# Kernel optimization log

Hardware: AMD Instinct MI355X
Metric: run time of the kernel (lower is better)

The kernel has to match this reference:

```python
import jax, jax.numpy as jnp
import numpy as np


def _bilinear_align_corners(img, H_out, W_out):
    # img: [B, C, h, w] -> [B, C, H_out, W_out], matching F.interpolate(mode='bilinear', align_corners=True)
    b, c, h, w = img.shape
    ys = jnp.linspace(0.0, h - 1.0, H_out)
    xs = jnp.linspace(0.0, w - 1.0, W_out)
    y0 = jnp.floor(ys).astype(jnp.int32)
    x0 = jnp.floor(xs).astype(jnp.int32)
    y1 = jnp.minimum(y0 + 1, h - 1)
    x1 = jnp.minimum(x0 + 1, w - 1)
    wy = (ys - y0)[:, None]          # [H_out, 1]
    wx = (xs - x0)[None, :]          # [1, W_out]

    def gather(yi, xi):
        return img[:, :, yi, :][:, :, :, xi]  # [B, C, H_out, W_out]

    top = gather(y0, x0) * (1.0 - wx) + gather(y0, x1) * wx
    bot = gather(y1, x0) * (1.0 - wx) + gather(y1, x1) * wx
    return top * (1.0 - wy) + bot * wy


def _conv1x1(x, W, b):
    # x: [B, C, H, W_], W: [O, C], b: [O]
    return jnp.einsum('bchw,oc->bohw', x, W) + b[None, :, None, None]


def setup_inputs() -> dict:
    key = jax.random.key(0)
    ks = jax.random.split(key, 9)
    B, C, H, W = 4, 256, 64, 64
    C8 = C // 8
    s_qk = 1.0 / np.sqrt(C)
    return {
        'x': jax.random.normal(ks[0], (B, C, H, W), dtype=jnp.float32),
        'guiding_map0': jax.random.normal(ks[1], (B, 1, 32, 32), dtype=jnp.float32),
        'Wq': jax.random.normal(ks[2], (C8, C), dtype=jnp.float32) * s_qk,
        'bq': jax.random.normal(ks[3], (C8,), dtype=jnp.float32) * 0.01,
        'Wk': jax.random.normal(ks[4], (C8, C), dtype=jnp.float32) * s_qk,
        'bk': jax.random.normal(ks[5], (C8,), dtype=jnp.float32) * 0.01,
        'Wv': jax.random.normal(ks[6], (C, C), dtype=jnp.float32) * s_qk,
        'bv': jax.random.normal(ks[7], (C,), dtype=jnp.float32) * 0.01,
        'gamma': jax.random.normal(ks[8], (1,), dtype=jnp.float32) * 0.1,
    }


def reference(x, guiding_map0, Wq, bq, Wk, bk, Wv, bv, gamma):
    B, C, H, W = x.shape
    N = H * W
    # upsample guiding map to x's spatial size, then sigmoid gate
    gm = jax.nn.sigmoid(_bilinear_align_corners(guiding_map0, H, W))  # [B,1,H,W]
    gate = 1.0 + gm

    q = (_conv1x1(x, Wq, bq) * gate).reshape(B, -1, N)  # [B, C//8, N]
    k = (_conv1x1(x, Wk, bk) * gate).reshape(B, -1, N)  # [B, C//8, N]
    v = (_conv1x1(x, Wv, bv) * gate).reshape(B, C, N)   # [B, C, N]

    # energy[b, n, m] = q[b, :, n] . k[b, :, m]
    energy = jnp.einsum('bcn,bcm->bnm', q, k)           # [B, N, N]
    attention = jax.nn.softmax(energy, axis=-1)
    # out[b, c, n] = sum_m v[b, c, m] * attention[b, n, m]
    out = jnp.einsum('bcm,bnm->bcn', v, attention).reshape(B, C, H, W)
    return gamma[0] * out + x
```

## Files before the change

kernel.cpp:

```cpp
#include <hip/hip_runtime.h>
#include <hip/hip_bf16.h>
#include <cstdint>

typedef __attribute__((ext_vector_type(4)))  float f32x4;
typedef __attribute__((ext_vector_type(16))) float f32x16;
typedef __attribute__((ext_vector_type(8)))  short s16x8;

#define LOG2E 1.4426950408889634f
#define RESC_THR 8.0f

#define B_   4
#define C_   256
#define N_   4096
#define NT_  256
#define MB_  128
#define QG_  128

#define WS_WFRAG 0u
#define WS_BIAS  163840u
#define WS_Q     262144u
#define WS_K     1310720u
#define WS_V     2359296u

__device__ __forceinline__ short bf16s(float f) {
  return (short)__bfloat16_as_ushort(__float2bfloat16(f));
}

__global__ void wprep_kernel(const float* __restrict__ Wq, const float* __restrict__ Wk,
                             const float* __restrict__ Wv, const float* __restrict__ bq,
                             const float* __restrict__ bk, const float* __restrict__ bv,
                             short* __restrict__ wfrag, float* __restrict__ bias) {
  int d0 = blockIdx.x * 256 + threadIdx.x;
  int d = d0;
  int j  = d & 7;  d >>= 3;
  int c  = d & 15; d >>= 4;
  int g  = d & 3;  d >>= 2;
  int ks = d & 7;  d >>= 3;
  int t  = d;
  int o  = t * 16 + c;
  int ch = ks * 32 + g * 8 + j;
  float w = (o < 32) ? Wq[o * 256 + ch] : (o < 64) ? Wk[(o - 32) * 256 + ch]
                                                   : Wv[(o - 64) * 256 + ch];
  wfrag[d0] = bf16s(w);
  if (d0 < 320) bias[d0] = (d0 < 32) ? bq[d0] : (d0 < 64) ? bk[d0 - 32] : bv[d0 - 64];
}

__global__ __launch_bounds__(256) void proj_kernel(
    const float* __restrict__ x, const short* __restrict__ wfrag,
    const float* __restrict__ bias, const float* __restrict__ gm,
    short* __restrict__ qs, short* __restrict__ ksz, short* __restrict__ vs) {
  int b = blockIdx.x >> 8, nt = blockIdx.x & 255;
  int lane = threadIdx.x & 63, wave = threadIdx.x >> 6;
  int g = lane >> 4, c = lane & 15;
  int n = nt * 16 + c;

  float gt;
  {
    int y = n >> 6, xp = n & 63;
    float fy = (float)(y * 31) / 63.0f;
    float fx = (float)(xp * 31) / 63.0f;
    int y0 = (int)fy, x0 = (int)fx;
    float wy = fy - (float)y0, wx = fx - (float)x0;
    int y1 = min(y0 + 1, 31), x1 = min(x0 + 1, 31);
    const float* p = gm + b * 1024;
    float v00 = p[y0 * 32 + x0], v01 = p[y0 * 32 + x1];
    float v10 = p[y1 * 32 + x0], v11 = p[y1 * 32 + x1];
    float top = v00 * (1.f - wx) + v01 * wx;
    float bot = v10 * (1.f - wx) + v11 * wx;
    float gv  = top * (1.f - wy) + bot * wy;
    gt = 1.0f + 1.0f / (1.0f + expf(-gv));
  }

  const float* xb = x + b * (C_ * N_) + n;
  s16x8 xf[8];
  #pragma unroll
  for (int ks = 0; ks < 8; ++ks) {
    int ch0 = ks * 32 + g * 8;
    s16x8 v;
    #pragma unroll
    for (int j = 0; j < 8; ++j) v[j] = bf16s(xb[(ch0 + j) * N_]);
    xf[ks] = v;
  }

  int qt32 = n >> 5, r = n & 31;
  for (int t = wave * 5; t < wave * 5 + 5; ++t) {
    f32x4 acc = {0.f, 0.f, 0.f, 0.f};
    #pragma unroll
    for (int ks = 0; ks < 8; ++ks) {
      s16x8 wf = *(const s16x8*)(wfrag + ((((t * 8 + ks) * 4 + g) * 16 + c) * 8));
      acc = __builtin_amdgcn_mfma_f32_16x16x32_bf16(wf, xf[ks], acc, 0, 0, 0);
    }
    #pragma unroll
    for (int jj = 0; jj < 4; ++jj) {
      int o = t * 16 + g * 4 + jj;
      float val = (acc[jj] + bias[o]) * gt;
      short bv16 = bf16s(val);
      if (o < 64) {
        int ch = o & 31;
        int s  = (ch >> 4) & 1, hi = (ch >> 3) & 1, j = ch & 7;
        short* dst = (o < 32) ? qs : ksz;
        dst[(((b * QG_ + qt32) * 2 + s) * 64 + hi * 32 + r) * 8 + j] = bv16;
      } else {
        int cv = o - 64;
        int ct = cv >> 5, lam = cv & 31;
        int s  = (r >> 4) & 1, r4 = r & 15;
        int k  = (r4 & 3) | (((r4 >> 3) & 1) << 2) | (((r4 >> 2) & 1) << 3);
        int hi = k >> 3, j = k & 7;
        vs[((((size_t)(b * MB_ + qt32) * 8 + ct) * 2 + s) * 64 + hi * 32 + lam) * 8 + j] = bv16;
      }
    }
  }
}

__global__ __launch_bounds__(256, 2) void attn_kernel(
    const short* __restrict__ qs, const short* __restrict__ ksz,
    const short* __restrict__ vs, const float* __restrict__ x,
    const float* __restrict__ gamma, float* __restrict__ out) {
  __shared__ float comb_m[4][32];
  __shared__ float comb_l[4][32];
  __shared__ float sumbuf[4][16][4][64];

  int bid = blockIdx.x;
  int b  = (bid & 7) >> 1;
  int qg = ((bid >> 3) << 1) | (bid & 1);
  int tid = threadIdx.x, lane = tid & 63, wave = tid >> 6;
  int lq = lane & 31;

  const short* qb = qs + (size_t)(((b * QG_ + qg) * 2) * 64 + lane) * 8;
  s16x8 qf0 = *(const s16x8*)(qb);
  s16x8 qf1 = *(const s16x8*)(qb + 512);

  f32x16 acc[8];
  #pragma unroll
  for (int ct = 0; ct < 8; ++ct)
    #pragma unroll
    for (int e = 0; e < 16; ++e) acc[ct][e] = 0.f;
  float m = -3.0e38f, lsum = 0.f;

  const short* kb0 = ksz + (size_t)b * (MB_ * 1024) + lane * 8;
  const short* vb0 = vs  + (size_t)b * ((size_t)MB_ * 8192) + lane * 8;

  int mb = wave;
  s16x8 kf0 = *(const s16x8*)(kb0 + mb * 1024);
  s16x8 kf1 = *(const s16x8*)(kb0 + mb * 1024 + 512);

  for (int i = 0; i < 32; ++i) {
    const short* vb = vb0 + (size_t)mb * 8192;
    s16x8 vf[16];
    #pragma unroll
    for (int t = 0; t < 16; ++t) vf[t] = *(const s16x8*)(vb + t * 512);

    f32x16 st;
    #pragma unroll
    for (int e = 0; e < 16; ++e) st[e] = 0.f;
    st = __builtin_amdgcn_mfma_f32_32x32x16_bf16(kf0, qf0, st, 0, 0, 0);
    st = __builtin_amdgcn_mfma_f32_32x32x16_bf16(kf1, qf1, st, 0, 0, 0);

    int mbn = (i < 31) ? (mb + 4) : wave;
    s16x8 nk0 = *(const s16x8*)(kb0 + mbn * 1024);
    s16x8 nk1 = *(const s16x8*)(kb0 + mbn * 1024 + 512);

    float pm = st[0];
    #pragma unroll
    for (int e = 1; e < 16; ++e) pm = fmaxf(pm, st[e]);
    pm = fmaxf(pm, __shfl_xor(pm, 32));

    if (!__all(pm <= m + RESC_THR)) {
      float mnew = fmaxf(m, pm);
      float scale = exp2f((m - mnew) * LOG2E);
      lsum *= scale;
      #pragma unroll
      for (int ct = 0; ct < 8; ++ct)
        #pragma unroll
        for (int e = 0; e < 16; ++e) acc[ct][e] *= scale;
      m = mnew;
    }

    float psum = 0.f;
    s16x8 pf0, pf1;
    #pragma unroll
    for (int j = 0; j < 8; ++j) {
      float p = exp2f((st[j] - m) * LOG2E);
      psum += p; pf0[j] = bf16s(p);
    }
    #pragma unroll
    for (int j = 0; j < 8; ++j) {
      float p = exp2f((st[8 + j] - m) * LOG2E);
      psum += p; pf1[j] = bf16s(p);
    }
    psum += __shfl_xor(psum, 32);
    lsum += psum;

    #pragma unroll
    for (int ct = 0; ct < 8; ++ct) {
      acc[ct] = __builtin_amdgcn_mfma_f32_32x32x16_bf16(vf[ct * 2],     pf0, acc[ct], 0, 0, 0);
      acc[ct] = __builtin_amdgcn_mfma_f32_32x32x16_bf16(vf[ct * 2 + 1], pf1, acc[ct], 0, 0, 0);
    }
    kf0 = nk0; kf1 = nk1; mb = mbn;
  }

  if (lane < 32) { comb_m[wave][lq] = m; comb_l[wave][lq] = lsum; }
  __syncthreads();
  float M = fmaxf(fmaxf(comb_m[0][lq], comb_m[1][lq]),
                  fmaxf(comb_m[2][lq], comb_m[3][lq]));
  float L = 0.f;
  #pragma unroll
  for (int w2 = 0; w2 < 4; ++w2)
    L += comb_l[w2][lq] * exp2f((comb_m[w2][lq] - M) * LOG2E);
  float myscale = exp2f((m - M) * LOG2E);
  float rn = gamma[0] / L;
  int n = qg * 32 + lq;
  int hi = lane >> 5;

  for (int phase = 0; phase < 2; ++phase) {
    #pragma unroll
    for (int t = 0; t < 4; ++t) {
      #pragma unroll
      for (int e = 0; e < 16; ++e)
        sumbuf[t][e][wave][lane] = acc[phase * 4 + t][e] * myscale;
    }
    __syncthreads();
    int ct = phase * 4 + wave;
    #pragma unroll
    for (int e = 0; e < 16; ++e) {
      float ssum = sumbuf[wave][e][0][lane] + sumbuf[wave][e][1][lane]
                 + sumbuf[wave][e][2][lane] + sumbuf[wave][e][3][lane];
      int ch = ct * 32 + (e & 3) + 8 * (e >> 2) + 4 * hi;
      int idx = (b * C_ + ch) * N_ + n;
      out[idx] = rn * ssum + x[idx];
    }
    __syncthreads();
  }
}

extern "C" void kernel_launch(void* const* d_in, const int* in_sizes, int n_in,
                              void* d_out, int out_size, void* d_ws, size_t ws_size,
                              hipStream_t stream) {
  const float* x     = (const float*)d_in[0];
  const float* gm    = (const float*)d_in[1];
  const float* Wq    = (const float*)d_in[2];
  const float* bq    = (const float*)d_in[3];
  const float* Wk    = (const float*)d_in[4];
  const float* bk    = (const float*)d_in[5];
  const float* Wv    = (const float*)d_in[6];
  const float* bv    = (const float*)d_in[7];
  const float* gamma = (const float*)d_in[8];

  char*  ws    = (char*)d_ws;
  short* wfrag = (short*)(ws + WS_WFRAG);
  float* bias  = (float*)(ws + WS_BIAS);
  short* qs    = (short*)(ws + WS_Q);
  short* ksz   = (short*)(ws + WS_K);
  short* vs    = (short*)(ws + WS_V);
  float* out   = (float*)d_out;

  wprep_kernel<<<dim3(320), dim3(256), 0, stream>>>(Wq, Wk, Wv, bq, bk, bv, wfrag, bias);
  proj_kernel<<<dim3(1024), dim3(256), 0, stream>>>(x, wfrag, bias, gm, qs, ksz, vs);
  attn_kernel<<<dim3(512), dim3(256), 0, stream>>>(qs, ksz, vs, x, gamma, out);
}
```

Measured before the change: 89.85 us.

## Process two query tiles per 512-thread block with software-pipelined V loads

Attention blocks grow to 8 waves covering two 32-query tiles, halving the grid. Waves sharing a key block sit in lockstep behind a per-iteration barrier, so their K/V fetches can hit in cache together. The first half of V for the next key block is prefetched into registers while the current block's second half is consumed, overlapping global loads with MFMA work. The epilogue reduction is reworked for the 8-wave split. The risks are higher register pressure under launch_bounds(512,2), barrier stalls, and a grid of only 256 blocks.

```diff
diff --git a/kernel.cpp b/kernel.cpp
--- a/kernel.cpp
+++ b/kernel.cpp
@@ -112,19 +112,21 @@
   }
 }
 
-__global__ __launch_bounds__(256, 2) void attn_kernel(
+__global__ __launch_bounds__(512, 2) void attn_kernel(
     const short* __restrict__ qs, const short* __restrict__ ksz,
     const short* __restrict__ vs, const float* __restrict__ x,
     const float* __restrict__ gamma, float* __restrict__ out) {
-  __shared__ float comb_m[4][32];
-  __shared__ float comb_l[4][32];
-  __shared__ float sumbuf[4][16][4][64];
+  __shared__ float comb_m[8][32];
+  __shared__ float comb_l[8][32];
+  __shared__ float sumbuf[16][16][64];
 
   int bid = blockIdx.x;
   int b  = (bid & 7) >> 1;
-  int qg = ((bid >> 3) << 1) | (bid & 1);
+  int qp = ((bid >> 3) << 1) | (bid & 1);
   int tid = threadIdx.x, lane = tid & 63, wave = tid >> 6;
-  int lq = lane & 31;
+  int qi = wave & 1, s = wave >> 1;
+  int qg = qp * 2 + qi;
+  int lq = lane & 31, hi = lane >> 5;
 
   const short* qb = qs + (size_t)(((b * QG_ + qg) * 2) * 64 + lane) * 8;
   s16x8 qf0 = *(const s16x8*)(qb);
@@ -140,15 +142,21 @@
   const short* kb0 = ksz + (size_t)b * (MB_ * 1024) + lane * 8;
   const short* vb0 = vs  + (size_t)b * ((size_t)MB_ * 8192) + lane * 8;
 
-  int mb = wave;
+  int mb = s;
   s16x8 kf0 = *(const s16x8*)(kb0 + mb * 1024);
   s16x8 kf1 = *(const s16x8*)(kb0 + mb * 1024 + 512);
+  s16x8 va[8];
+  {
+    const short* vb = vb0 + (size_t)mb * 8192;
+    #pragma unroll
+    for (int t = 0; t < 8; ++t) va[t] = *(const s16x8*)(vb + t * 512);
+  }
 
   for (int i = 0; i < 32; ++i) {
     const short* vb = vb0 + (size_t)mb * 8192;
-    s16x8 vf[16];
-    #pragma unroll
-    for (int t = 0; t < 16; ++t) vf[t] = *(const s16x8*)(vb + t * 512);
+    s16x8 vb2[8];
+    #pragma unroll
+    for (int t = 0; t < 8; ++t) vb2[t] = *(const s16x8*)(vb + (8 + t) * 512);
 
     f32x16 st;
     #pragma unroll
@@ -156,7 +164,7 @@
     st = __builtin_amdgcn_mfma_f32_32x32x16_bf16(kf0, qf0, st, 0, 0, 0);
     st = __builtin_amdgcn_mfma_f32_32x32x16_bf16(kf1, qf1, st, 0, 0, 0);
 
-    int mbn = (i < 31) ? (mb + 4) : wave;
+    int mbn = (i < 31) ? (mb + 4) : s;
     s16x8 nk0 = *(const s16x8*)(kb0 + mbn * 1024);
     s16x8 nk1 = *(const s16x8*)(kb0 + mbn * 1024 + 512);
 
@@ -192,42 +200,55 @@
     lsum += psum;
 
     #pragma unroll
-    for (int ct = 0; ct < 8; ++ct) {
-      acc[ct] = __builtin_amdgcn_mfma_f32_32x32x16_bf16(vf[ct * 2],     pf0, acc[ct], 0, 0, 0);
-      acc[ct] = __builtin_amdgcn_mfma_f32_32x32x16_bf16(vf[ct * 2 + 1], pf1, acc[ct], 0, 0, 0);
+    for (int ct = 0; ct < 4; ++ct) {
+      acc[ct] = __builtin_amdgcn_mfma_f32_32x32x16_bf16(va[ct * 2],     pf0, acc[ct], 0, 0, 0);
+      acc[ct] = __builtin_amdgcn_mfma_f32_32x32x16_bf16(va[ct * 2 + 1], pf1, acc[ct], 0, 0, 0);
+    }
+    {
+      const short* vbn = vb0 + (size_t)mbn * 8192;
+      #pragma unroll
+      for (int t = 0; t < 8; ++t) va[t] = *(const s16x8*)(vbn + t * 512);
+    }
+    #pragma unroll
+    for (int ct = 4; ct < 8; ++ct) {
+      acc[ct] = __builtin_amdgcn_mfma_f32_32x32x16_bf16(vb2[(ct - 4) * 2],     pf0, acc[ct], 0, 0, 0);
+      acc[ct] = __builtin_amdgcn_mfma_f32_32x32x16_bf16(vb2[(ct - 4) * 2 + 1], pf1, acc[ct], 0, 0, 0);
     }
     kf0 = nk0; kf1 = nk1; mb = mbn;
+    __builtin_amdgcn_s_barrier();
   }
 
   if (lane < 32) { comb_m[wave][lq] = m; comb_l[wave][lq] = lsum; }
   __syncthreads();
-  float M = fmaxf(fmaxf(comb_m[0][lq], comb_m[1][lq]),
-                  fmaxf(comb_m[2][lq], comb_m[3][lq]));
+  float M = fmaxf(fmaxf(comb_m[qi][lq], comb_m[2 + qi][lq]),
+                  fmaxf(comb_m[4 + qi][lq], comb_m[6 + qi][lq]));
   float L = 0.f;
   #pragma unroll
-  for (int w2 = 0; w2 < 4; ++w2)
-    L += comb_l[w2][lq] * exp2f((comb_m[w2][lq] - M) * LOG2E);
+  for (int s2 = 0; s2 < 4; ++s2)
+    L += comb_l[s2 * 2 + qi][lq] * exp2f((comb_m[s2 * 2 + qi][lq] - M) * LOG2E);
   float myscale = exp2f((m - M) * LOG2E);
   float rn = gamma[0] / L;
   int n = qg * 32 + lq;
-  int hi = lane >> 5;
-
-  for (int phase = 0; phase < 2; ++phase) {
-    #pragma unroll
-    for (int t = 0; t < 4; ++t) {
+
+  for (int p = 0; p < 4; ++p) {
+    #pragma unroll
+    for (int t = 0; t < 2; ++t) {
       #pragma unroll
       for (int e = 0; e < 16; ++e)
-        sumbuf[t][e][wave][lane] = acc[phase * 4 + t][e] * myscale;
+        sumbuf[(qi * 2 + t) * 4 + s][e][lane] = acc[p * 2 + t][e] * myscale;
     }
     __syncthreads();
-    int ct = phase * 4 + wave;
-    #pragma unroll
-    for (int e = 0; e < 16; ++e) {
-      float ssum = sumbuf[wave][e][0][lane] + sumbuf[wave][e][1][lane]
-                 + sumbuf[wave][e][2][lane] + sumbuf[wave][e][3][lane];
-      int ch = ct * 32 + (e & 3) + 8 * (e >> 2) + 4 * hi;
-      int idx = (b * C_ + ch) * N_ + n;
-      out[idx] = rn * ssum + x[idx];
+    if (s < 2) {
+      int slot = (qi * 2 + s) * 4;
+      int ct = p * 2 + s;
+      #pragma unroll
+      for (int e = 0; e < 16; ++e) {
+        float ssum = sumbuf[slot][e][lane] + sumbuf[slot + 1][e][lane]
+                   + sumbuf[slot + 2][e][lane] + sumbuf[slot + 3][e][lane];
+        int ch = ct * 32 + (e & 3) + 8 * (e >> 2) + 4 * hi;
+        int idx = (b * C_ + ch) * N_ + n;
+        out[idx] = rn * ssum + x[idx];
+      }
     }
     __syncthreads();
   }
@@ -256,5 +277,5 @@
 
   wprep_kernel<<<dim3(320), dim3(256), 0, stream>>>(Wq, Wk, Wv, bq, bk, bv, wfrag, bias);
   proj_kernel<<<dim3(1024), dim3(256), 0, stream>>>(x, wfrag, bias, gm, qs, ksz, vs);
-  attn_kernel<<<dim3(512), dim3(256), 0, stream>>>(qs, ksz, vs, x, gamma, out);
-}
+  attn_kernel<<<dim3(256), dim3(512), 0, stream>>>(qs, ksz, vs, x, gamma, out);
+}
```

Result: no change. 88.96 us (-1.0%).

## Split attention over key blocks with LDS-shared K/V and separate combine kernel

Applied to the files above, without the earlier changes.

Replaces the per-wave register-streamed attention with a split-K scheme. Each 512-thread block handles 8 query tiles that share K/V tiles, double-buffered in LDS through global_load_lds, over a quarter of the key range. The block writes bf16 partial outputs plus per-row max and sum to workspace, and a new combine kernel merges the four splits and adds the residual. The goal is to cut redundant global K/V traffic by reusing it across waves, at the cost of an extra kernel launch, partial-result round trips through memory, and bf16 rounding of partial accumulators. The split path runs only when the workspace is large enough, otherwise it falls back to the old kernel.

```diff
diff --git a/kernel.cpp b/kernel.cpp
--- a/kernel.cpp
+++ b/kernel.cpp
@@ -21,9 +21,21 @@
 #define WS_Q     262144u
 #define WS_K     1310720u
 #define WS_V     2359296u
+#define WS_PART  11534336u
+#define WS_ML    45088768u
+#define WS_NEED  45613056ull
 
 __device__ __forceinline__ short bf16s(float f) {
   return (short)__bfloat16_as_ushort(__float2bfloat16(f));
+}
+__device__ __forceinline__ float bf2f(short h) {
+  union { unsigned u; float f; } v; v.u = ((unsigned)(unsigned short)h) << 16;
+  return v.f;
+}
+__device__ __forceinline__ void gl_lds16(const void* g, void* l) {
+  __builtin_amdgcn_global_load_lds(
+      (const __attribute__((address_space(1))) unsigned int*)g,
+      (__attribute__((address_space(3))) unsigned int*)l, 16, 0, 0);
 }
 
 __global__ void wprep_kernel(const float* __restrict__ Wq, const float* __restrict__ Wk,
@@ -112,7 +124,156 @@
   }
 }
 
-__global__ __launch_bounds__(256, 2) void attn_kernel(
+__global__ __launch_bounds__(512, 2) void attn_split_kernel(
+    const short* __restrict__ qs, const short* __restrict__ ksz,
+    const short* __restrict__ vs, short* __restrict__ part,
+    float* __restrict__ mlbuf) {
+  __shared__ __align__(16) short k_lds[2][1024];
+  __shared__ __align__(16) short v_lds[2][8192];
+
+  int bid = blockIdx.x;
+  int b  = (bid & 7) >> 1;
+  int u  = ((bid >> 3) << 1) | (bid & 1);
+  int qb = u >> 2, s = u & 3;
+  int tid = threadIdx.x, lane = tid & 63, wave = tid >> 6;
+  int lq = lane & 31, hi = lane >> 5;
+  int qt = qb * 8 + wave;
+
+  const short* qbp = qs + (size_t)(((b * QG_ + qt) * 2) * 64 + lane) * 8;
+  s16x8 qf0 = *(const s16x8*)(qbp);
+  s16x8 qf1 = *(const s16x8*)(qbp + 512);
+
+  f32x16 acc[8];
+  #pragma unroll
+  for (int ct = 0; ct < 8; ++ct)
+    #pragma unroll
+    for (int e = 0; e < 16; ++e) acc[ct][e] = 0.f;
+  float m = -3.0e38f, lsum = 0.f;
+
+  const char* kbase = (const char*)(ksz + (size_t)b * (MB_ * 1024));
+  const char* vbase = (const char*)(vs + (size_t)b * ((size_t)MB_ * 8192));
+
+  #define STAGE(mb, nb)                                                          \
+    {                                                                            \
+      const char* vsrc = vbase + (size_t)(mb) * 16384;                           \
+      gl_lds16(vsrc + (wave * 2 + 0) * 1024 + lane * 16,                         \
+               &v_lds[nb][(wave * 2 + 0) * 512]);                                \
+      gl_lds16(vsrc + (wave * 2 + 1) * 1024 + lane * 16,                         \
+               &v_lds[nb][(wave * 2 + 1) * 512]);                                \
+      if (wave < 2) {                                                            \
+        const char* ksrc = kbase + (size_t)(mb) * 2048;                          \
+        gl_lds16(ksrc + wave * 1024 + lane * 16, &k_lds[nb][wave * 512]);        \
+      }                                                                          \
+    }
+
+  STAGE(s * 32, 0);
+  __syncthreads();
+
+  for (int i = 0; i < 32; ++i) {
+    int cur = i & 1;
+    if (i < 31) STAGE(s * 32 + i + 1, cur ^ 1);
+
+    const short* kb = k_lds[cur];
+    s16x8 kf0 = *(const s16x8*)(kb + lane * 8);
+    s16x8 kf1 = *(const s16x8*)(kb + 512 + lane * 8);
+    f32x16 st;
+    #pragma unroll
+    for (int e = 0; e < 16; ++e) st[e] = 0.f;
+    st = __builtin_amdgcn_mfma_f32_32x32x16_bf16(kf0, qf0, st, 0, 0, 0);
+    st = __builtin_amdgcn_mfma_f32_32x32x16_bf16(kf1, qf1, st, 0, 0, 0);
+
+    float pm = st[0];
+    #pragma unroll
+    for (int e = 1; e < 16; ++e) pm = fmaxf(pm, st[e]);
+    pm = fmaxf(pm, __shfl_xor(pm, 32));
+
+    if (!__all(pm <= m + RESC_THR)) {
+      float mnew = fmaxf(m, pm);
+      float scale = exp2f((m - mnew) * LOG2E);
+      lsum *= scale;
+      #pragma unroll
+      for (int ct = 0; ct < 8; ++ct)
+        #pragma unroll
+        for (int e = 0; e < 16; ++e) acc[ct][e] *= scale;
+      m = mnew;
+    }
+
+    float psum = 0.f;
+    s16x8 pf0, pf1;
+    #pragma unroll
+    for (int j = 0; j < 8; ++j) {
+      float p = exp2f((st[j] - m) * LOG2E);
+      psum += p; pf0[j] = bf16s(p);
+    }
+    #pragma unroll
+    for (int j = 0; j < 8; ++j) {
+      float p = exp2f((st[8 + j] - m) * LOG2E);
+      psum += p; pf1[j] = bf16s(p);
+    }
+    psum += __shfl_xor(psum, 32);
+    lsum += psum;
+
+    const short* vb = v_lds[cur];
+    #pragma unroll
+    for (int ct = 0; ct < 8; ++ct) {
+      s16x8 vf0 = *(const s16x8*)(vb + (ct * 2 + 0) * 512 + lane * 8);
+      s16x8 vf1 = *(const s16x8*)(vb + (ct * 2 + 1) * 512 + lane * 8);
+      acc[ct] = __builtin_amdgcn_mfma_f32_32x32x16_bf16(vf0, pf0, acc[ct], 0, 0, 0);
+      acc[ct] = __builtin_amdgcn_mfma_f32_32x32x16_bf16(vf1, pf1, acc[ct], 0, 0, 0);
+    }
+    __syncthreads();
+  }
+
+  int pt = (b * 128 + qt) * 4 + s;
+  if (lane < 32) {
+    mlbuf[pt * 64 + lq]      = m;
+    mlbuf[pt * 64 + 32 + lq] = lsum;
+  }
+  short* pb = part + (size_t)pt * 8192;
+  #pragma unroll
+  for (int ct = 0; ct < 8; ++ct)
+    #pragma unroll
+    for (int e = 0; e < 16; ++e) {
+      int CH = ct * 32 + (e & 3) + 8 * (e >> 2) + 4 * hi;
+      pb[CH * 32 + lq] = bf16s(acc[ct][e]);
+    }
+  #undef STAGE
+}
+
+__global__ __launch_bounds__(256) void combine_kernel(
+    const short* __restrict__ part, const float* __restrict__ mlbuf,
+    const float* __restrict__ x, const float* __restrict__ gamma,
+    float* __restrict__ out) {
+  int bid = blockIdx.x;
+  int b = bid >> 7, qt = bid & 127;
+  int t = threadIdx.x;
+  int q = t & 31, cg = t >> 5;
+  int base = (b * 128 + qt) * 4;
+  float m0 = mlbuf[(base + 0) * 64 + q], m1 = mlbuf[(base + 1) * 64 + q];
+  float m2 = mlbuf[(base + 2) * 64 + q], m3 = mlbuf[(base + 3) * 64 + q];
+  float M = fmaxf(fmaxf(m0, m1), fmaxf(m2, m3));
+  float w0 = exp2f((m0 - M) * LOG2E), w1 = exp2f((m1 - M) * LOG2E);
+  float w2 = exp2f((m2 - M) * LOG2E), w3 = exp2f((m3 - M) * LOG2E);
+  float L = mlbuf[(base + 0) * 64 + 32 + q] * w0 + mlbuf[(base + 1) * 64 + 32 + q] * w1
+          + mlbuf[(base + 2) * 64 + 32 + q] * w2 + mlbuf[(base + 3) * 64 + 32 + q] * w3;
+  float rn = gamma[0] / L;
+  int n = qt * 32 + q;
+  const short* p0 = part + (size_t)(base + 0) * 8192;
+  const short* p1 = part + (size_t)(base + 1) * 8192;
+  const short* p2 = part + (size_t)(base + 2) * 8192;
+  const short* p3 = part + (size_t)(base + 3) * 8192;
+  #pragma unroll 4
+  for (int cc = 0; cc < 32; ++cc) {
+    int ch = cg * 32 + cc;
+    int off = ch * 32 + q;
+    float o = w0 * bf2f(p0[off]) + w1 * bf2f(p1[off])
+            + w2 * bf2f(p2[off]) + w3 * bf2f(p3[off]);
+    int idx = (b * C_ + ch) * N_ + n;
+    out[idx] = rn * o + x[idx];
+  }
+}
+
+__global__ __launch_bounds__(256, 2) void attn_reg_kernel(
     const short* __restrict__ qs, const short* __restrict__ ksz,
     const short* __restrict__ vs, const float* __restrict__ x,
     const float* __restrict__ gamma, float* __restrict__ out) {
@@ -214,11 +375,10 @@
 
   for (int phase = 0; phase < 2; ++phase) {
     #pragma unroll
-    for (int t = 0; t < 4; ++t) {
+    for (int t = 0; t < 4; ++t)
       #pragma unroll
       for (int e = 0; e < 16; ++e)
         sumbuf[t][e][wave][lane] = acc[phase * 4 + t][e] * myscale;
-    }
     __syncthreads();
     int ct = phase * 4 + wave;
     #pragma unroll
@@ -256,5 +416,13 @@
 
   wprep_kernel<<<dim3(320), dim3(256), 0, stream>>>(Wq, Wk, Wv, bq, bk, bv, wfrag, bias);
   proj_kernel<<<dim3(1024), dim3(256), 0, stream>>>(x, wfrag, bias, gm, qs, ksz, vs);
-  attn_kernel<<<dim3(512), dim3(256), 0, stream>>>(qs, ksz, vs, x, gamma, out);
-}
+
+  if (ws_size >= WS_NEED) {
+    short* part  = (short*)(ws + WS_PART);
+    float* mlbuf = (float*)(ws + WS_ML);
+    attn_split_kernel<<<dim3(256), dim3(512), 0, stream>>>(qs, ksz, vs, part, mlbuf);
+    combine_kernel<<<dim3(512), dim3(256), 0, stream>>>(part, mlbuf, x, gamma, out);
+  } else {
+    attn_reg_kernel<<<dim3(512), dim3(256), 0, stream>>>(qs, ksz, vs, x, gamma, out);
+  }
+}
```

After: 94.87 us. 1.06x slower.
